# Kernel tuning notes

Hardware: AMD Instinct MI355X
Metric: run time of the kernel (lower is better)

Reference implementation:

```python
import jax, jax.numpy as jnp
import numpy as np

B, T, P, H, E, K, COND = 4096, 20, 20, 256, 128, 5, 5
CTX = E + H + P  # embedded condition + encoder hidden + time-stamp one-hot-cumsum


def setup_inputs():
    key = jax.random.key(0)
    ks = jax.random.split(key, 12)
    g = lambda k, sh, s=0.05: (jax.random.normal(k, sh) * s).astype(jnp.float32)
    return dict(
        conditions=g(ks[0], (B, T, COND), 1.0),
        state_h=g(ks[1], (B, H), 0.1),
        state_c=g(ks[2], (B, H), 0.1),
        steps_n=T,
        We1=g(ks[3], (COND, E)), be1=jnp.zeros((E,), jnp.float32),
        We2=g(ks[4], (E, E)), be2=jnp.zeros((E,), jnp.float32),
        Wk=g(ks[5], (CTX, 4 * H)), Wr=g(ks[6], (H, 4 * H)), bl=jnp.zeros((4 * H,), jnp.float32),
        Wm=g(ks[7], (H, 6 * K)), bm=jnp.zeros((6 * K,), jnp.float32),
        Wy=g(ks[8], (H, 3 * K)), by=jnp.zeros((3 * K,), jnp.float32),
        Wf=g(ks[9], (H, 3 * K)), bf=jnp.zeros((3 * K,), jnp.float32),
        Wfadj=g(ks[10], (H, 3 * K)), bfadj=jnp.zeros((3 * K,), jnp.float32),
    )


def _decode(conditions, state_h, state_c, steps_n, We1, be1, We2, be2,
            Wk, Wr, bl, Wm, bm, Wy, by, Wf, bf, Wfadj, bfadj):
    Bn = conditions.shape[0]
    enc_h = state_h  # reshaped encoder hidden, concatenated into context every step
    base_key = jax.random.key(42)

    def lstm_step(x):
        # Keras gate order i,f,c,o. NOTE: original resets initial_state=self.state
        # (never updated) so every step starts from the encoder state -- kept faithful.
        z = x @ Wk + state_h @ Wr + bl
        i, f, g, o = jnp.split(z, 4, axis=-1)
        c = jax.nn.sigmoid(f) * state_c + jax.nn.sigmoid(i) * jnp.tanh(g)
        return jax.nn.sigmoid(o) * jnp.tanh(c)

    def head_other(h, W, b, k):
        # univariate GMM head: [softmax alphas | mus | exp sigmas], plus one sample
        p = h @ W + b
        logits, mu, ls = jnp.split(p, 3, axis=-1)
        alphas, sig = jax.nn.softmax(logits, axis=-1), jnp.exp(ls)
        vec = jnp.concatenate([alphas, mu, sig], axis=-1)
        k1, k2 = jax.random.split(k)
        idx = jax.random.categorical(k1, logits)[:, None]
        mu_k = jnp.take_along_axis(mu, idx, 1)
        s_k = jnp.take_along_axis(sig, idx, 1)
        return vec, mu_k + s_k * jax.random.normal(k2, mu_k.shape)

    def step(carry, i):
        cond, key = carry
        key, km, ky, kf, kfa = jax.random.split(key, 5)
        emb = (cond @ We1 + be1) @ We2 + be2  # fc_embedding: two linear Dense layers
        ts = (jnp.arange(P) <= i).astype(cond.dtype)  # cumulative time stamp (faithful)
        ctx = jnp.concatenate([emb, enc_h, jnp.broadcast_to(ts, (Bn, P))], axis=-1)
        h = lstm_step(ctx)
        # merge vehicle: bivariate correlated GMM
        pm = h @ Wm + bm
        logits, mu_lo, ls_lo, mu_la, ls_la, rr = jnp.split(pm, 6, axis=-1)
        alphas = jax.nn.softmax(logits, axis=-1)
        s_lo, s_la, rho = jnp.exp(ls_lo), jnp.exp(ls_la), jnp.tanh(rr)
        vec_m = jnp.concatenate([alphas, mu_lo, s_lo, mu_la, s_la, rho], axis=-1)
        k1, k2 = jax.random.split(km)
        idx = jax.random.categorical(k1, logits)[:, None]
        take = lambda a: jnp.take_along_axis(a, idx, 1)
        z = jax.random.normal(k2, (Bn, 2))
        x_lo = take(mu_lo) + take(s_lo) * z[:, :1]
        r = take(rho)
        x_la = take(mu_la) + take(s_la) * (r * z[:, :1] + jnp.sqrt(1.0 - r * r) * z[:, 1:])
        vec_y, s_y = head_other(h, Wy, by, ky)
        vec_f, s_f = head_other(h, Wf, bf, kf)
        vec_fa, s_fa = head_other(h, Wfadj, bfadj, kfa)
        new_cond = jnp.concatenate([x_lo, x_la, s_y, s_f, s_fa], axis=-1)  # [B,5]
        return (new_cond, key), (vec_m, vec_y, vec_f, vec_fa)

    init = (conditions[:, 0, :], base_key)
    _, (vm, vy, vf, vfa) = jax.lax.scan(step, init, jnp.arange(steps_n))
    tr = lambda a: jnp.transpose(a, (1, 0, 2))  # [T,B,D] -> [B,T,D]
    return tr(vm), tr(vy), tr(vf), tr(vfa)


def reference(conditions, state_h, state_c, steps_n, We1, be1, We2, be2,
              Wk, Wr, bl, Wm, bm, Wy, by, Wf, bf, Wfadj, bfadj):
    # returns the concatenated GMM parameter sequences for (merge, yield, f, fadj)
    return _decode(conditions, state_h, state_c, steps_n, We1, be1, We2, be2,
                   Wk, Wr, bl, Wm, bm, Wy, by, Wf, bf, Wfadj, bfadj)
```

## Files before the change

### kernel.cpp

```cpp
#include <hip/hip_runtime.h>
#include <stdint.h>
#include <math.h>

#define BN 4096
#define TT 20
#define HH 256
#define EE 128
#define KK 5
#define NCOND 5

#define WS_TSC  512
#define WS_WTB  20992
#define WS_BIAS 41472
#define WS_ZC   42320
#define WS_M    43344
#define WS_WSUM 48464
#define WS_CZ   560608
#define WS_END  (WS_CZ + BN*1024)

#define PSTR 84

#define TINYF 1.17549435e-38f
#define LO_N  0.99999994f
#define LOG2E 1.44269504f
#define LN2   0.69314718f

typedef __attribute__((ext_vector_type(8))) short short8v;
typedef __attribute__((ext_vector_type(4))) float f32x4;

__device__ __host__ __forceinline__ constexpr void tf2(
    uint32_t k0, uint32_t k1, uint32_t x0, uint32_t x1, uint32_t& o0, uint32_t& o1) {
  const uint32_t ks2 = k0 ^ k1 ^ 0x1BD11BDAu;
  x0 += k0; x1 += k1;
#define RND(r) { x0 += x1; x1 = (x1 << (r)) | (x1 >> (32 - (r))); x1 ^= x0; }
  RND(13) RND(15) RND(26) RND(6)   x0 += k1;  x1 += ks2 + 1u;
  RND(17) RND(29) RND(16) RND(24)  x0 += ks2; x1 += k0 + 2u;
  RND(13) RND(15) RND(26) RND(6)   x0 += k0;  x1 += k1 + 3u;
  RND(17) RND(29) RND(16) RND(24)  x0 += k1;  x1 += ks2 + 4u;
  RND(13) RND(15) RND(26) RND(6)   x0 += ks2; x1 += k0 + 5u;
#undef RND
  o0 = x0; o1 = x1;
}

struct KeyTab { uint32_t v[TT * 16]; };
constexpr KeyTab mkkeys() {
  KeyTab kt{};
  uint32_t kx = 0u, ky = 42u;
  for (int t = 0; t < TT; ++t) {
    for (int l = 0; l < 4; ++l) {
      uint32_t hx = 0, hy = 0, a = 0, b = 0, c = 0, d = 0;
      tf2(kx, ky, 0u, (uint32_t)(l + 1), hx, hy);
      tf2(hx, hy, 0u, 0u, a, b);
      tf2(hx, hy, 0u, 1u, c, d);
      kt.v[t * 16 + l * 4 + 0] = a;
      kt.v[t * 16 + l * 4 + 1] = b;
      kt.v[t * 16 + l * 4 + 2] = c;
      kt.v[t * 16 + l * 4 + 3] = d;
    }
    uint32_t nx = 0, ny = 0;
    tf2(kx, ky, 0u, 0u, nx, ny);
    kx = nx; ky = ny;
  }
  return kt;
}
__constant__ KeyTab KT = mkkeys();

__device__ __forceinline__ uint32_t pbits(uint32_t k0, uint32_t k1, uint32_t n) {
  uint32_t a, b;
  tf2(k0, k1, 0u, n, a, b);
  return a ^ b;
}

__device__ __forceinline__ float u01f(uint32_t bits) {
  return __uint_as_float((bits >> 9) | 0x3f800000u) - 1.0f;
}

__device__ __forceinline__ float fexp(float x) { return __builtin_amdgcn_exp2f(x * LOG2E); }
__device__ __forceinline__ float flog(float x) { return __builtin_amdgcn_logf(x) * LN2; }
__device__ __forceinline__ float frcp(float x) { return __builtin_amdgcn_rcpf(x); }
__device__ __forceinline__ float fsig(float x) {
  return frcp(1.0f + __builtin_amdgcn_exp2f(-x * LOG2E));
}
__device__ __forceinline__ float ftanh(float x) {
  return 1.0f - 2.0f * frcp(1.0f + __builtin_amdgcn_exp2f(x * (2.0f * LOG2E)));
}

__device__ __forceinline__ float erfinv_f(float x) {
  float w = -flog(fmaf(-x, x, 1.0f));
  float p;
  if (w < 5.0f) {
    w = w - 2.5f;
    p = 2.81022636e-08f;
    p = 3.43273939e-07f + p * w;
    p = -3.5233877e-06f + p * w;
    p = -4.39150654e-06f + p * w;
    p = 0.00021858087f  + p * w;
    p = -0.00125372503f + p * w;
    p = -0.00417768164f + p * w;
    p = 0.246640727f    + p * w;
    p = 1.50140941f     + p * w;
  } else {
    w = sqrtf(w) - 3.0f;
    p = -0.000200214257f;
    p = 0.000100950558f + p * w;
    p = 0.00134934322f  + p * w;
    p = -0.00367342844f + p * w;
    p = 0.00573950773f  + p * w;
    p = -0.0076224613f  + p * w;
    p = 0.00943887047f  + p * w;
    p = 1.00167406f     + p * w;
    p = 2.83297682f     + p * w;
  }
  return p * x;
}

__device__ __forceinline__ uint32_t bf16rne(float f) {
  uint32_t u = __float_as_uint(f);
  return (u + 0x7fffu + ((u >> 16) & 1u)) >> 16;
}

#define RB_WSUM  0
#define RB_TSC   1024
#define RB_WTB   1028
#define RB_BIAS  1108
#define RB_MZC   1109
#define RB_TOT   1113
__global__ __launch_bounds__(256) void prep_misc(
    const float* __restrict__ Wk, const float* __restrict__ Wr,
    const float* __restrict__ We1, const float* __restrict__ be1,
    const float* __restrict__ We2, const float* __restrict__ be2,
    const float* __restrict__ Wm, const float* __restrict__ bm,
    const float* __restrict__ Wy, const float* __restrict__ by,
    const float* __restrict__ Wf, const float* __restrict__ bf,
    const float* __restrict__ Wfa, const float* __restrict__ bfa,
    const float* __restrict__ bl, float* __restrict__ ws) {
  __shared__ float smem[768];
  const int bid = blockIdx.x, tid = threadIdx.x;

  if (bid < RB_TSC) {
    const int idx = bid * 256 + tid;
    const int q = idx >> 10, col = idx & 1023;
    ws[WS_WSUM + idx] = Wk[(size_t)(EE + q) * 1024 + col] + Wr[(size_t)q * 1024 + col];
  } else if (bid < RB_WTB) {
    const int col = (bid - RB_TSC) * 256 + tid;
    float s = 0.0f;
    for (int p = 0; p < TT; ++p) {
      s += Wk[(size_t)(EE + HH + p) * 1024 + col];
      ws[WS_TSC + p * 1024 + col] = s;
    }
  } else if (bid < RB_BIAS) {
    const int idx = (bid - RB_WTB) * 256 + tid;
    const int o = idx >> 8, q = idx & 255;
    float v = 0.0f;
    if (o < 30)      v = Wm[q * 30 + o];
    else if (o < 45) v = Wy[q * 15 + (o - 30)];
    else if (o < 60) v = Wf[q * 15 + (o - 45)];
    else if (o < 75) v = Wfa[q * 15 + (o - 60)];
    uint16_t* wtb = (uint16_t*)&ws[WS_WTB];
    wtb[o * 256 + (q ^ ((o & 7) << 3))] = (uint16_t)bf16rne(v);
  } else if (bid == RB_BIAS) {
    if (tid < 80) {
      float v = 0.0f;
      if (tid < 30)      v = bm[tid];
      else if (tid < 45) v = by[tid - 30];
      else if (tid < 60) v = bf[tid - 45];
      else if (tid < 75) v = bfa[tid - 60];
      ws[WS_BIAS + tid] = v;
    }
  } else {
    float* T1s = smem;
    float* eb2s = smem + 640;
    if (tid < EE) {
      const int q = tid;
      float t0 = 0.f, t1 = 0.f, t2 = 0.f, t3 = 0.f, t4 = 0.f;
      float eb = be2[q];
      for (int e = 0; e < EE; ++e) {
        const float w2 = We2[e * EE + q];
        t0 = fmaf(We1[0 * EE + e], w2, t0);
        t1 = fmaf(We1[1 * EE + e], w2, t1);
        t2 = fmaf(We1[2 * EE + e], w2, t2);
        t3 = fmaf(We1[3 * EE + e], w2, t3);
        t4 = fmaf(We1[4 * EE + e], w2, t4);
        eb = fmaf(be1[e], w2, eb);
      }
      T1s[0 * 128 + q] = t0; T1s[1 * 128 + q] = t1; T1s[2 * 128 + q] = t2;
      T1s[3 * 128 + q] = t3; T1s[4 * 128 + q] = t4; eb2s[q] = eb;
    }
    __syncthreads();
    const int col = (bid - RB_MZC) * 256 + tid;
    float m0 = 0.f, m1 = 0.f, m2 = 0.f, m3 = 0.f, m4 = 0.f;
    float zacc = bl[col];
    for (int q = 0; q < EE; ++q) {
      const float wv = Wk[(size_t)q * 1024 + col];
      m0 = fmaf(T1s[0 * 128 + q], wv, m0);
      m1 = fmaf(T1s[1 * 128 + q], wv, m1);
      m2 = fmaf(T1s[2 * 128 + q], wv, m2);
      m3 = fmaf(T1s[3 * 128 + q], wv, m3);
      m4 = fmaf(T1s[4 * 128 + q], wv, m4);
      zacc = fmaf(eb2s[q], wv, zacc);
    }
    ws[WS_M + 0 * 1024 + col] = m0;
    ws[WS_M + 1 * 1024 + col] = m1;
    ws[WS_M + 2 * 1024 + col] = m2;
    ws[WS_M + 3 * 1024 + col] = m3;
    ws[WS_M + 4 * 1024 + col] = m4;
    ws[WS_ZC + col] = zacc;
  }
}

__global__ __launch_bounds__(512) void prep_czgemm(
    const float* __restrict__ state_h, float* __restrict__ ws) {
  __shared__ short Ab[128 * 256];
  __shared__ short Bb[128 * 256];
  const int tid = threadIdx.x;
  const int brow = blockIdx.x >> 3, bcol = blockIdx.x & 7;
  const int row0 = brow * 128, col0 = bcol * 128;

  for (int i = tid; i < 128 * 256; i += 512) {
    const int m = i >> 8, k = i & 255;
    Ab[m * 256 + (k ^ ((m & 7) << 3))] =
        (short)bf16rne(state_h[(size_t)(row0 + m) * HH + k]);
  }
  for (int i = tid; i < 128 * 256; i += 512) {
    const int k = i >> 7, n = i & 127;
    Bb[n * 256 + (k ^ ((n & 7) << 3))] =
        (short)bf16rne(ws[WS_WSUM + k * 1024 + col0 + n]);
  }
  __syncthreads();

  const int wv = tid >> 6, lane = tid & 63;
  const int wr = wv >> 2, wc = wv & 3;
  const int rc = lane & 15, hq = lane >> 4;
  f32x4 acc[4][2];
#pragma unroll
  for (int fr = 0; fr < 4; ++fr)
#pragma unroll
    for (int fc = 0; fc < 2; ++fc) acc[fr][fc] = (f32x4){0.f, 0.f, 0.f, 0.f};

#pragma unroll
  for (int kk = 0; kk < 8; ++kk) {
    const int kbase = kk * 32 + hq * 8;
    short8v av[4], bv[2];
#pragma unroll
    for (int fr = 0; fr < 4; ++fr) {
      const int m = wr * 64 + fr * 16 + rc;
      av[fr] = *(const short8v*)&Ab[m * 256 + (kbase ^ ((m & 7) << 3))];
    }
#pragma unroll
    for (int fc = 0; fc < 2; ++fc) {
      const int n = wc * 32 + fc * 16 + rc;
      bv[fc] = *(const short8v*)&Bb[n * 256 + (kbase ^ ((n & 7) << 3))];
    }
#pragma unroll
    for (int fr = 0; fr < 4; ++fr)
#pragma unroll
      for (int fc = 0; fc < 2; ++fc)
        acc[fr][fc] = __builtin_amdgcn_mfma_f32_16x16x32_bf16(av[fr], bv[fc],
                                                              acc[fr][fc], 0, 0, 0);
  }

#pragma unroll
  for (int fc = 0; fc < 2; ++fc) {
    const int colg = col0 + wc * 32 + fc * 16 + rc;
    const float zcv = ws[WS_ZC + colg];
#pragma unroll
    for (int fr = 0; fr < 4; ++fr) {
#pragma unroll
      for (int j = 0; j < 4; ++j) {
        const int row = row0 + wr * 64 + fr * 16 + hq * 4 + j;
        ws[WS_CZ + (size_t)row * 1024 + colg] = acc[fr][fc][j] + zcv;
      }
    }
  }
}

__global__ __launch_bounds__(512) void decode_main(
    const float* __restrict__ conditions, const float* __restrict__ state_h,
    const float* __restrict__ state_c, const float* __restrict__ ws,
    float* __restrict__ out, int use_cz) {
  __shared__ float Msh[5 * 1024];
  __shared__ short WTBs[80 * 256];
  __shared__ short hb[16 * 256];
  __shared__ float psh[8 * PSTR];
  __shared__ float biasL[80];
  __shared__ float conds[8 * 8];

  const int tid = threadIdx.x;
  const int row0 = blockIdx.x * 8;
  const int u = tid & 255;
  const int half = tid >> 8;
  const int rbase = half * 4;

  for (int i = tid; i < 5 * 1024; i += 512) Msh[i] = ws[WS_M + i];
  if (tid < 80) biasL[tid] = ws[WS_BIAS + tid];
  if (tid < 8 * NCOND) {
    const int r = tid / NCOND, c = tid - r * NCOND;
    conds[r * 8 + c] = conditions[(size_t)(row0 + r) * (TT * NCOND) + c];
  }
  float sc[4];
#pragma unroll
  for (int rr = 0; rr < 4; ++rr) sc[rr] = state_c[(size_t)(row0 + rbase + rr) * HH + u];

  const bool cth = (tid < 256);
  const int kci = tid & 7;
  const int rci = tid >> 5;
  const int headci = (tid >> 3) & 3;
  const int crow = row0 + rci;
  const int cbase2 = headci ? (30 + 15 * (headci - 1)) : 0;

  float cz[4][4];
  if (use_cz) {
#pragma unroll
    for (int g = 0; g < 4; ++g)
#pragma unroll
      for (int rr = 0; rr < 4; ++rr)
        cz[g][rr] = ws[WS_CZ + (size_t)(row0 + rbase + rr) * 1024 + g * 256 + u];
    {
      uint32_t* dst = (uint32_t*)WTBs;
      const uint32_t* src = (const uint32_t*)&ws[WS_WTB];
      for (int i = tid; i < 80 * 128; i += 512) dst[i] = src[i];
      uint32_t* hz = (uint32_t*)hb;
      for (int i = tid; i < 1024; i += 512) hz[1024 + i] = 0u;
    }
    __syncthreads();
  } else {
    float* hstage = (float*)WTBs;
    for (int i = tid; i < 8 * HH; i += 512) hstage[i] = state_h[(size_t)row0 * HH + i];
    __syncthreads();
#pragma unroll
    for (int g = 0; g < 4; ++g) {
      const float z = ws[WS_ZC + g * 256 + u];
#pragma unroll
      for (int rr = 0; rr < 4; ++rr) cz[g][rr] = z;
    }
    for (int q = 0; q < HH; ++q) {
      const float w0 = ws[WS_WSUM + q * 1024 + u];
      const float w1 = ws[WS_WSUM + q * 1024 + 256 + u];
      const float w2 = ws[WS_WSUM + q * 1024 + 512 + u];
      const float w3 = ws[WS_WSUM + q * 1024 + 768 + u];
#pragma unroll
      for (int rr = 0; rr < 4; ++rr) {
        const float e = hstage[(rbase + rr) * HH + q];
        cz[0][rr] = fmaf(e, w0, cz[0][rr]);
        cz[1][rr] = fmaf(e, w1, cz[1][rr]);
        cz[2][rr] = fmaf(e, w2, cz[2][rr]);
        cz[3][rr] = fmaf(e, w3, cz[3][rr]);
      }
    }
    __syncthreads();
    {
      uint32_t* dst = (uint32_t*)WTBs;
      const uint32_t* src = (const uint32_t*)&ws[WS_WTB];
      for (int i = tid; i < 80 * 128; i += 512) dst[i] = src[i];
      uint32_t* hz = (uint32_t*)hb;
      for (int i = tid; i < 1024; i += 512) hz[1024 + i] = 0u;
    }
    __syncthreads();
  }

  for (int t = 0; t < TT; ++t) {
    float pg = 0.0f, pz0 = 0.0f, pz1 = 0.0f, pzz = 0.0f;
    if (cth) {
      if (kci < 5) {
        float uu = u01f(pbits(KT.v[t * 16 + headci * 4 + 0],
                              KT.v[t * 16 + headci * 4 + 1],
                              (uint32_t)(crow * KK + kci)));
        uu = fmaxf(TINYF, uu * (1.0f - TINYF) + TINYF);
        pg = -flog(-flog(uu));
      }
      if (kci == 0) {
        if (headci == 0) {
          float u0 = u01f(pbits(KT.v[t * 16 + 2], KT.v[t * 16 + 3],
                                (uint32_t)(crow * 2))) * 2.0f - LO_N;
          float u1 = u01f(pbits(KT.v[t * 16 + 2], KT.v[t * 16 + 3],
                                (uint32_t)(crow * 2 + 1))) * 2.0f - LO_N;
          u0 = fmaxf(-LO_N, u0); u1 = fmaxf(-LO_N, u1);
          pz0 = 1.41421356f * erfinv_f(u0);
          pz1 = 1.41421356f * erfinv_f(u1);
        } else {
          float uz = u01f(pbits(KT.v[t * 16 + headci * 4 + 2],
                                KT.v[t * 16 + headci * 4 + 3],
                                (uint32_t)crow)) * 2.0f - LO_N;
          uz = fmaxf(-LO_N, uz);
          pzz = 1.41421356f * erfinv_f(uz);
        }
      }
    }
    {
      const float ts0 = ws[WS_TSC + t * 1024 + u];
      const float ts1 = ws[WS_TSC + t * 1024 + 256 + u];
      const float ts2 = ws[WS_TSC + t * 1024 + 512 + u];
      const float ts3 = ws[WS_TSC + t * 1024 + 768 + u];
      float mA[5], mB[5], mC[5], mD[5];
#pragma unroll
      for (int c = 0; c < 5; ++c) {
        mA[c] = Msh[c * 1024 + u];
        mB[c] = Msh[c * 1024 + 256 + u];
        mC[c] = Msh[c * 1024 + 512 + u];
        mD[c] = Msh[c * 1024 + 768 + u];
      }
#pragma unroll
      for (int rr = 0; rr < 4; ++rr) {
        const int row = rbase + rr;
        const float c0 = conds[row * 8 + 0], c1 = conds[row * 8 + 1], c2 = conds[row * 8 + 2],
                    c3 = conds[row * 8 + 3], c4 = conds[row * 8 + 4];
        float zi = cz[0][rr] + ts0, zf = cz[1][rr] + ts1,
              zg = cz[2][rr] + ts2, zo = cz[3][rr] + ts3;
        zi = fmaf(c0, mA[0], zi); zi = fmaf(c1, mA[1], zi); zi = fmaf(c2, mA[2], zi);
        zi = fmaf(c3, mA[3], zi); zi = fmaf(c4, mA[4], zi);
        zf = fmaf(c0, mB[0], zf); zf = fmaf(c1, mB[1], zf); zf = fmaf(c2, mB[2], zf);
        zf = fmaf(c3, mB[3], zf); zf = fmaf(c4, mB[4], zf);
        zg = fmaf(c0, mC[0], zg); zg = fmaf(c1, mC[1], zg); zg = fmaf(c2, mC[2], zg);
        zg = fmaf(c3, mC[3], zg); zg = fmaf(c4, mC[4], zg);
        zo = fmaf(c0, mD[0], zo); zo = fmaf(c1, mD[1], zo); zo = fmaf(c2, mD[2], zo);
        zo = fmaf(c3, mD[3], zo); zo = fmaf(c4, mD[4], zo);
        const float cv = fsig(zf) * sc[rr] + fsig(zi) * ftanh(zg);
        const float hv = fsig(zo) * ftanh(cv);
        hb[row * 256 + (u ^ ((row & 7) << 3))] = (short)bf16rne(hv);
      }
    }
    __syncthreads();
    {
      const int wv = tid >> 6;
      if (wv < 5) {
        const int lane = tid & 63;
        const int rc = lane & 15;
        const int hq = lane >> 4;
        const int nn = wv * 16 + rc;
        const int aswz = (rc & 7) << 3;
        const int bswz = (nn & 7) << 3;
        f32x4 acc = {0.0f, 0.0f, 0.0f, 0.0f};
#pragma unroll
        for (int kk = 0; kk < 8; ++kk) {
          const int kbase = kk * 32 + hq * 8;
          const short8v av = *(const short8v*)&hb[rc * 256 + (kbase ^ aswz)];
          const short8v bv = *(const short8v*)&WTBs[nn * 256 + (kbase ^ bswz)];
          acc = __builtin_amdgcn_mfma_f32_16x16x32_bf16(av, bv, acc, 0, 0, 0);
        }
        if (hq < 2) {
#pragma unroll
          for (int j = 0; j < 4; ++j) {
            const int prow = hq * 4 + j;
            psh[prow * PSTR + nn] = acc[j] + biasL[nn];
          }
        }
      }
    }
    __syncthreads();
    if (cth) {
      const float lk = (kci < 5) ? psh[rci * PSTR + cbase2 + kci] : -INFINITY;
      float mx = fmaxf(lk, __shfl_xor(lk, 1));
      mx = fmaxf(mx, __shfl_xor(mx, 2));
      mx = fmaxf(mx, __shfl_xor(mx, 4));
      const float ek = (kci < 5) ? fexp(lk - mx) : 0.0f;
      float ss = ek + __shfl_xor(ek, 1);
      ss += __shfl_xor(ss, 2);
      ss += __shfl_xor(ss, 4);
      const float rss = frcp(ss);
      float v = -INFINITY;
      if (kci < 5) v = lk + pg;
      float vm = fmaxf(v, __shfl_xor(v, 1));
      vm = fmaxf(vm, __shfl_xor(vm, 2));
      vm = fmaxf(vm, __shfl_xor(vm, 4));
      int cand = (v == vm) ? kci : 8;
      cand = min(cand, __shfl_xor(cand, 1));
      cand = min(cand, __shfl_xor(cand, 2));
      cand = min(cand, __shfl_xor(cand, 4));
      const int idx = cand;
      const size_t ob = headci
          ? ((size_t)BN * TT * 30 + (size_t)(headci - 1) * BN * TT * 15 +
             ((size_t)crow * TT + t) * 15)
          : ((size_t)crow * TT + t) * 30;
      if (kci < 5) {
        out[ob + kci] = ek * rss;
        out[ob + 5 + kci] = psh[rci * PSTR + cbase2 + 5 + kci];
        out[ob + 10 + kci] = fexp(psh[rci * PSTR + cbase2 + 10 + kci]);
        if (headci == 0) {
          out[ob + 15 + kci] = psh[rci * PSTR + 15 + kci];
          out[ob + 20 + kci] = fexp(psh[rci * PSTR + 20 + kci]);
          out[ob + 25 + kci] = ftanh(psh[rci * PSTR + 25 + kci]);
        }
      }
      if (kci == 0) {
        if (headci == 0) {
          const float mu = psh[rci * PSTR + 5 + idx];
          const float sl = fexp(psh[rci * PSTR + 10 + idx]);
          const float mula = psh[rci * PSTR + 15 + idx];
          const float sla = fexp(psh[rci * PSTR + 20 + idx]);
          const float rho = ftanh(psh[rci * PSTR + 25 + idx]);
          conds[rci * 8 + 0] = mu + sl * pz0;
          conds[rci * 8 + 1] = mula + sla * (rho * pz0 + sqrtf(1.0f - rho * rho) * pz1);
        } else {
          conds[rci * 8 + 1 + headci] =
              psh[rci * PSTR + cbase2 + 5 + idx] +
              fexp(psh[rci * PSTR + cbase2 + 10 + idx]) * pzz;
        }
      }
    }
    __syncthreads();
  }
}

extern "C" void kernel_launch(void* const* d_in, const int* in_sizes, int n_in,
                              void* d_out, int out_size, void* d_ws, size_t ws_size,
                              hipStream_t stream) {
  const float* conditions = (const float*)d_in[0];
  const float* state_h = (const float*)d_in[1];
  const float* state_c = (const float*)d_in[2];
  const float* We1 = (const float*)d_in[4];
  const float* be1 = (const float*)d_in[5];
  const float* We2 = (const float*)d_in[6];
  const float* be2 = (const float*)d_in[7];
  const float* Wk  = (const float*)d_in[8];
  const float* Wr  = (const float*)d_in[9];
  const float* bl  = (const float*)d_in[10];
  const float* Wm  = (const float*)d_in[11];
  const float* bm  = (const float*)d_in[12];
  const float* Wy  = (const float*)d_in[13];
  const float* by  = (const float*)d_in[14];
  const float* Wf  = (const float*)d_in[15];
  const float* bf  = (const float*)d_in[16];
  const float* Wfa = (const float*)d_in[17];
  const float* bfa = (const float*)d_in[18];
  float* ws = (float*)d_ws;
  float* out = (float*)d_out;

  const int use_cz = (ws_size >= (size_t)WS_END * 4) ? 1 : 0;

  prep_misc<<<dim3(RB_TOT), dim3(256), 0, stream>>>(
      Wk, Wr, We1, be1, We2, be2, Wm, bm, Wy, by, Wf, bf, Wfa, bfa, bl, ws);
  if (use_cz) {
    prep_czgemm<<<dim3(256), dim3(512), 0, stream>>>(state_h, ws);
  }
  decode_main<<<dim3(BN / 8), dim3(512), 0, stream>>>(
      conditions, state_h, state_c, ws, out, use_cz);
}
```

Baseline: 125.9 us.

## Precompute next step's random draws on idle waves during MFMA head phase

Per-step Gumbel and normal random generation moves out of the critical path. Threads 320+ (the waves not doing MFMA head work) compute step t+1's values into double-buffered shared memory while the other waves run the head matmul, and step 0 is generated before the loop. This shortens the serial per-step dependency chain at the cost of extra shared memory and a more complex buffer indexing scheme.

```diff
diff --git a/kernel.cpp b/kernel.cpp
--- a/kernel.cpp
+++ b/kernel.cpp
@@ -119,6 +119,34 @@
   return (u + 0x7fffu + ((u >> 16) & 1u)) >> 16;
 }
 
+__device__ __forceinline__ void gen_rng_step(
+    int tt, int row0, int jj, float (*rngG)[4][KK], float (*rngN)[5]) {
+  if (jj < 160) {
+    const int r = jj / 20, rest = jj % 20, hd = rest / 5, k = rest % 5;
+    const int rw = row0 + r;
+    float uu = u01f(pbits(KT.v[tt * 16 + hd * 4 + 0], KT.v[tt * 16 + hd * 4 + 1],
+                          (uint32_t)(rw * KK + k)));
+    uu = fmaxf(TINYF, uu * (1.0f - TINYF) + TINYF);
+    rngG[r][hd][k] = -flog(-flog(uu));
+  } else {
+    for (int slot = jj - 160; slot < 40; slot += 32) {
+      const int r = slot / 5, s = slot % 5;
+      const int rw = row0 + r;
+      float uz;
+      if (s < 2) {
+        uz = u01f(pbits(KT.v[tt * 16 + 2], KT.v[tt * 16 + 3],
+                        (uint32_t)(rw * 2 + s))) * 2.0f - LO_N;
+      } else {
+        const int hd = s - 1;
+        uz = u01f(pbits(KT.v[tt * 16 + hd * 4 + 2], KT.v[tt * 16 + hd * 4 + 3],
+                        (uint32_t)rw)) * 2.0f - LO_N;
+      }
+      uz = fmaxf(-LO_N, uz);
+      rngN[r][s] = 1.41421356f * erfinv_f(uz);
+    }
+  }
+}
+
 #define RB_WSUM  0
 #define RB_TSC   1024
 #define RB_WTB   1028
@@ -284,6 +312,8 @@
   __shared__ float psh[8 * PSTR];
   __shared__ float biasL[80];
   __shared__ float conds[8 * 8];
+  __shared__ float rngG[2][8][4][KK];
+  __shared__ float rngN[2][8][5];
 
   const int tid = threadIdx.x;
   const int row0 = blockIdx.x * 8;
@@ -307,6 +337,8 @@
   const int headci = (tid >> 3) & 3;
   const int crow = row0 + rci;
   const int cbase2 = headci ? (30 + 15 * (headci - 1)) : 0;
+
+  if (tid >= 320) gen_rng_step(0, row0, tid - 320, rngG[0], rngN[0]);
 
   float cz[4][4];
   if (use_cz) {
@@ -359,33 +391,7 @@
   }
 
   for (int t = 0; t < TT; ++t) {
-    float pg = 0.0f, pz0 = 0.0f, pz1 = 0.0f, pzz = 0.0f;
-    if (cth) {
-      if (kci < 5) {
-        float uu = u01f(pbits(KT.v[t * 16 + headci * 4 + 0],
-                              KT.v[t * 16 + headci * 4 + 1],
-                              (uint32_t)(crow * KK + kci)));
-        uu = fmaxf(TINYF, uu * (1.0f - TINYF) + TINYF);
-        pg = -flog(-flog(uu));
-      }
-      if (kci == 0) {
-        if (headci == 0) {
-          float u0 = u01f(pbits(KT.v[t * 16 + 2], KT.v[t * 16 + 3],
-                                (uint32_t)(crow * 2))) * 2.0f - LO_N;
-          float u1 = u01f(pbits(KT.v[t * 16 + 2], KT.v[t * 16 + 3],
-                                (uint32_t)(crow * 2 + 1))) * 2.0f - LO_N;
-          u0 = fmaxf(-LO_N, u0); u1 = fmaxf(-LO_N, u1);
-          pz0 = 1.41421356f * erfinv_f(u0);
-          pz1 = 1.41421356f * erfinv_f(u1);
-        } else {
-          float uz = u01f(pbits(KT.v[t * 16 + headci * 4 + 2],
-                                KT.v[t * 16 + headci * 4 + 3],
-                                (uint32_t)crow)) * 2.0f - LO_N;
-          uz = fmaxf(-LO_N, uz);
-          pzz = 1.41421356f * erfinv_f(uz);
-        }
-      }
-    }
+    const int pcur = t & 1;
     {
       const float ts0 = ws[WS_TSC + t * 1024 + u];
       const float ts1 = ws[WS_TSC + t * 1024 + 256 + u];
@@ -444,6 +450,8 @@
             psh[prow * PSTR + nn] = acc[j] + biasL[nn];
           }
         }
+      } else if (t + 1 < TT) {
+        gen_rng_step(t + 1, row0, tid - 320, rngG[pcur ^ 1], rngN[pcur ^ 1]);
       }
     }
     __syncthreads();
@@ -458,7 +466,7 @@
       ss += __shfl_xor(ss, 4);
       const float rss = frcp(ss);
       float v = -INFINITY;
-      if (kci < 5) v = lk + pg;
+      if (kci < 5) v = lk + rngG[pcur][rci][headci][kci];
       float vm = fmaxf(v, __shfl_xor(v, 1));
       vm = fmaxf(vm, __shfl_xor(vm, 2));
       vm = fmaxf(vm, __shfl_xor(vm, 4));
@@ -483,6 +491,8 @@
       }
       if (kci == 0) {
         if (headci == 0) {
+          const float pz0 = rngN[pcur][rci][0];
+          const float pz1 = rngN[pcur][rci][1];
           const float mu = psh[rci * PSTR + 5 + idx];
           const float sl = fexp(psh[rci * PSTR + 10 + idx]);
           const float mula = psh[rci * PSTR + 15 + idx];
@@ -491,6 +501,7 @@
           conds[rci * 8 + 0] = mu + sl * pz0;
           conds[rci * 8 + 1] = mula + sla * (rho * pz0 + sqrtf(1.0f - rho * rho) * pz1);
         } else {
+          const float pzz = rngN[pcur][rci][1 + headci];
           conds[rci * 8 + 1 + headci] =
               psh[rci * PSTR + cbase2 + 5 + idx] +
               fexp(psh[rci * PSTR + cbase2 + 10 + idx]) * pzz;
```

New measurement: 130.3 us. 1.03x slower.
